# Kernel optimization log

Hardware: AMD Instinct MI355X
Metric: run time of the kernel (lower is better)

## Reference

```python
import jax, jax.numpy as jnp
import numpy as np
from jax import lax

IN_CH, HID, OUT_CH, N_MID, BATCH = 16, 8, 4, 60, 4194304


def setup_inputs() -> dict:
    key = jax.random.key(0)
    ks = jax.random.split(key, 7)
    scale = 1.0 / jnp.sqrt(jnp.float32(HID))  # keep 62-layer linear chain numerically stable
    x = jax.random.normal(ks[0], (BATCH, IN_CH), dtype=jnp.float32)
    W1 = jax.random.normal(ks[1], (HID, IN_CH), dtype=jnp.float32) * scale
    b1 = jax.random.normal(ks[2], (HID,), dtype=jnp.float32) * 0.01
    Ws = jax.random.normal(ks[3], (N_MID, HID, HID), dtype=jnp.float32) * scale
    bs = jax.random.normal(ks[4], (N_MID, HID), dtype=jnp.float32) * 0.01
    W2 = jax.random.normal(ks[5], (OUT_CH, HID), dtype=jnp.float32) * scale
    b2 = jax.random.normal(ks[6], (OUT_CH,), dtype=jnp.float32) * 0.01
    return {"x": x, "W1": W1, "b1": b1, "Ws": Ws, "bs": bs, "W2": W2, "b2": b2}


def reference(x, W1, b1, Ws, bs, W2, b2):
    # fc1: [B,16] -> [B,8]  (torch Linear: x @ W.T + b)
    h = x @ W1.T + b1

    # 60 sequential 8x8 Linear layers, no activation; scan over layer axis
    def step(h, wb):
        w, b = wb
        return h @ w.T + b, None

    h, _ = lax.scan(step, h, (Ws, bs))

    # fc2: [B,8] -> [B,4]
    return h @ W2.T + b2
```

## Files before the change

### kernel.cpp

```cpp
#include <hip/hip_runtime.h>

#define IN_CH  16
#define HID    8
#define OUT_CH 4
#define N_MID  60
#define BATCH  4194304

__global__ __launch_bounds__(128) void fold_kernel(
    const float* __restrict__ W1, const float* __restrict__ b1,
    const float* __restrict__ Ws, const float* __restrict__ bs,
    const float* __restrict__ W2, const float* __restrict__ b2,
    float* __restrict__ Mc ) {

    __shared__ float sWs[N_MID * HID * HID];
    __shared__ float sbs[N_MID * HID];
    __shared__ float A[2][HID][IN_CH];
    __shared__ float d[2][HID];

    const int t   = threadIdx.x;
    const int r   = t >> 4;
    const int col = t & 15;

    for (int i = t; i < N_MID * HID * HID; i += 128) sWs[i] = Ws[i];
    for (int i = t; i < N_MID * HID;       i += 128) sbs[i] = bs[i];

    A[0][r][col] = W1[r * IN_CH + col];
    if (t < HID) d[0][t] = b1[t];
    __syncthreads();

    int cur = 0;
    for (int l = 0; l < N_MID; ++l) {
        const float* W = sWs + l * HID * HID;
        float acc = 0.f;
        #pragma unroll
        for (int k = 0; k < HID; ++k)
            acc += W[r * HID + k] * A[cur][k][col];
        A[1 - cur][r][col] = acc;
        if (t < HID) {
            float bc = sbs[l * HID + t];
            #pragma unroll
            for (int k = 0; k < HID; ++k)
                bc += W[t * HID + k] * d[cur][k];
            d[1 - cur][t] = bc;
        }
        cur = 1 - cur;
        __syncthreads();
    }

    if (t < OUT_CH * IN_CH) {
        const int rr = t >> 4, cc = t & 15;
        float acc = 0.f;
        #pragma unroll
        for (int k = 0; k < HID; ++k)
            acc += W2[rr * HID + k] * A[cur][k][cc];
        Mc[rr * IN_CH + cc] = acc;
    }
    if (t < OUT_CH) {
        float acc = b2[t];
        #pragma unroll
        for (int k = 0; k < HID; ++k)
            acc += W2[t * HID + k] * d[cur][k];
        Mc[OUT_CH * IN_CH + t] = acc;
    }
}

__global__ __launch_bounds__(256) void apply_kernel(
    const float* __restrict__ x,
    const float* __restrict__ Mc,
    float* __restrict__ out) {

    const int tid = threadIdx.x;
    const size_t g = (size_t)blockIdx.x * 256 + tid;
    const int q = tid & 3;

    const float4* M4 = (const float4*)Mc;
    const float4 m0 = M4[0 * 4 + q];
    const float4 m1 = M4[1 * 4 + q];
    const float4 m2 = M4[2 * 4 + q];
    const float4 m3 = M4[3 * 4 + q];
    const float  cb = Mc[OUT_CH * IN_CH + q];

    const float4 xv = ((const float4*)x)[g];

    float p0 = m0.x * xv.x + m0.y * xv.y + m0.z * xv.z + m0.w * xv.w;
    float p1 = m1.x * xv.x + m1.y * xv.y + m1.z * xv.z + m1.w * xv.w;
    float p2 = m2.x * xv.x + m2.y * xv.y + m2.z * xv.z + m2.w * xv.w;
    float p3 = m3.x * xv.x + m3.y * xv.y + m3.z * xv.z + m3.w * xv.w;

    p0 += __shfl_xor(p0, 1); p1 += __shfl_xor(p1, 1);
    p2 += __shfl_xor(p2, 1); p3 += __shfl_xor(p3, 1);
    p0 += __shfl_xor(p0, 2); p1 += __shfl_xor(p1, 2);
    p2 += __shfl_xor(p2, 2); p3 += __shfl_xor(p3, 2);

    const float val = (q == 0 ? p0 : q == 1 ? p1 : q == 2 ? p2 : p3) + cb;
    out[g] = val;
}

extern "C" void kernel_launch(void* const* d_in, const int* in_sizes, int n_in,
                              void* d_out, int out_size, void* d_ws, size_t ws_size,
                              hipStream_t stream) {
    const float* x  = (const float*)d_in[0];
    const float* W1 = (const float*)d_in[1];
    const float* b1 = (const float*)d_in[2];
    const float* Ws = (const float*)d_in[3];
    const float* bs = (const float*)d_in[4];
    const float* W2 = (const float*)d_in[5];
    const float* b2 = (const float*)d_in[6];
    float* out = (float*)d_out;
    float* Mc  = (float*)d_ws;

    fold_kernel<<<1, 128, 0, stream>>>(W1, b1, Ws, bs, W2, b2, Mc);

    const int blocks = (BATCH * (IN_CH / 4)) / 256;
    apply_kernel<<<blocks, 256, 0, stream>>>(x, Mc, out);
}
```

Measured before the change: 396.0 us.

## Batch loads per thread, use nontemporal memory ops, reduce shuffles, shrink fold block

The apply kernel now handles 8 float4 elements per thread, spaced by a grid-wide stride, and issues all of their loads up front to keep more memory traffic in flight. Loads and stores use nontemporal hints so the streaming data does not pollute the cache. The shuffle reduction is replaced by a butterfly exchange-and-select scheme that needs 3 shuffles instead of 8. The fold kernel shrinks to a single 64-thread wavefront that copies weights to shared memory with float4 loads and computes two rows per thread; this cuts occupancy headroom but removes cross-wave synchronisation cost.

Result: no change. 395.6 us (-0.1%).

```diff
diff --git a/kernel.cpp b/kernel.cpp
--- a/kernel.cpp
+++ b/kernel.cpp
@@ -6,7 +6,9 @@
 #define N_MID  60
 #define BATCH  4194304
 
-__global__ __launch_bounds__(128) void fold_kernel(
+typedef float vfloat4 __attribute__((ext_vector_type(4)));
+
+__global__ __launch_bounds__(64) void fold_kernel(
     const float* __restrict__ W1, const float* __restrict__ b1,
     const float* __restrict__ Ws, const float* __restrict__ bs,
     const float* __restrict__ W2, const float* __restrict__ b2,
@@ -18,36 +20,49 @@
     __shared__ float d[2][HID];
 
     const int t   = threadIdx.x;
-    const int r   = t >> 4;
     const int col = t & 15;
+    const int r0  = t >> 4;
 
-    for (int i = t; i < N_MID * HID * HID; i += 128) sWs[i] = Ws[i];
-    for (int i = t; i < N_MID * HID;       i += 128) sbs[i] = bs[i];
+    {
+        const float4* Ws4  = (const float4*)Ws;
+        float4*       sW4  = (float4*)sWs;
+        #pragma unroll 1
+        for (int i = t; i < N_MID * HID * HID / 4; i += 64) sW4[i] = Ws4[i];
+        const float4* bs4  = (const float4*)bs;
+        float4*       sb4  = (float4*)sbs;
+        for (int i = t; i < N_MID * HID / 4; i += 64) sb4[i] = bs4[i];
+    }
 
-    A[0][r][col] = W1[r * IN_CH + col];
+    A[0][r0][col]     = W1[r0 * IN_CH + col];
+    A[0][r0 + 4][col] = W1[(r0 + 4) * IN_CH + col];
     if (t < HID) d[0][t] = b1[t];
     __syncthreads();
 
     int cur = 0;
     for (int l = 0; l < N_MID; ++l) {
         const float* W = sWs + l * HID * HID;
-        float acc = 0.f;
+        float a0 = 0.f, a1 = 0.f;
         #pragma unroll
-        for (int k = 0; k < HID; ++k)
-            acc += W[r * HID + k] * A[cur][k][col];
-        A[1 - cur][r][col] = acc;
+        for (int k = 0; k < HID; ++k) {
+            const float av = A[cur][k][col];
+            a0 += W[r0 * HID + k]       * av;
+            a1 += W[(r0 + 4) * HID + k] * av;
+        }
+        float bc = 0.f;
         if (t < HID) {
-            float bc = sbs[l * HID + t];
+            bc = sbs[l * HID + t];
             #pragma unroll
             for (int k = 0; k < HID; ++k)
                 bc += W[t * HID + k] * d[cur][k];
-            d[1 - cur][t] = bc;
         }
-        cur = 1 - cur;
+        A[1 - cur][r0][col]     = a0;
+        A[1 - cur][r0 + 4][col] = a1;
+        if (t < HID) d[1 - cur][t] = bc;
+        cur ^= 1;
         __syncthreads();
     }
 
-    if (t < OUT_CH * IN_CH) {
+    {
         const int rr = t >> 4, cc = t & 15;
         float acc = 0.f;
         #pragma unroll
@@ -64,14 +79,15 @@
     }
 }
 
+#define ITERS 8
+
 __global__ __launch_bounds__(256) void apply_kernel(
     const float* __restrict__ x,
     const float* __restrict__ Mc,
     float* __restrict__ out) {
 
     const int tid = threadIdx.x;
-    const size_t g = (size_t)blockIdx.x * 256 + tid;
-    const int q = tid & 3;
+    const int q   = tid & 3;
 
     const float4* M4 = (const float4*)Mc;
     const float4 m0 = M4[0 * 4 + q];
@@ -80,20 +96,38 @@
     const float4 m3 = M4[3 * 4 + q];
     const float  cb = Mc[OUT_CH * IN_CH + q];
 
-    const float4 xv = ((const float4*)x)[g];
+    const vfloat4* __restrict__ x4 = (const vfloat4*)x;
+    const size_t g0     = (size_t)blockIdx.x * 256 + tid;
+    const size_t stride = (size_t)gridDim.x * 256;
 
-    float p0 = m0.x * xv.x + m0.y * xv.y + m0.z * xv.z + m0.w * xv.w;
-    float p1 = m1.x * xv.x + m1.y * xv.y + m1.z * xv.z + m1.w * xv.w;
-    float p2 = m2.x * xv.x + m2.y * xv.y + m2.z * xv.z + m2.w * xv.w;
-    float p3 = m3.x * xv.x + m3.y * xv.y + m3.z * xv.z + m3.w * xv.w;
+    vfloat4 xv[ITERS];
+    #pragma unroll
+    for (int j = 0; j < ITERS; ++j)
+        xv[j] = __builtin_nontemporal_load(&x4[g0 + j * stride]);
 
-    p0 += __shfl_xor(p0, 1); p1 += __shfl_xor(p1, 1);
-    p2 += __shfl_xor(p2, 1); p3 += __shfl_xor(p3, 1);
-    p0 += __shfl_xor(p0, 2); p1 += __shfl_xor(p1, 2);
-    p2 += __shfl_xor(p2, 2); p3 += __shfl_xor(p3, 2);
+    const bool hi2 = (q & 2) != 0;
+    const bool lo1 = (q & 1) != 0;
 
-    const float val = (q == 0 ? p0 : q == 1 ? p1 : q == 2 ? p2 : p3) + cb;
-    out[g] = val;
+    #pragma unroll
+    for (int j = 0; j < ITERS; ++j) {
+        const vfloat4 v = xv[j];
+        float p0 = m0.x * v.x + m0.y * v.y + m0.z * v.z + m0.w * v.w;
+        float p1 = m1.x * v.x + m1.y * v.y + m1.z * v.z + m1.w * v.w;
+        float p2 = m2.x * v.x + m2.y * v.y + m2.z * v.z + m2.w * v.w;
+        float p3 = m3.x * v.x + m3.y * v.y + m3.z * v.z + m3.w * v.w;
+
+        float send_a = hi2 ? p0 : p2;
+        float send_b = hi2 ? p1 : p3;
+        float recv_a = __shfl_xor(send_a, 2);
+        float recv_b = __shfl_xor(send_b, 2);
+        float k0 = (hi2 ? p2 : p0) + recv_a;
+        float k1 = (hi2 ? p3 : p1) + recv_b;
+        float send = lo1 ? k0 : k1;
+        float recv = __shfl_xor(send, 1);
+        float val  = (lo1 ? k1 : k0) + recv + cb;
+
+        __builtin_nontemporal_store(val, &out[g0 + j * stride]);
+    }
 }
 
 extern "C" void kernel_launch(void* const* d_in, const int* in_sizes, int n_in,
@@ -109,8 +143,8 @@
     float* out = (float*)d_out;
     float* Mc  = (float*)d_ws;
 
-    fold_kernel<<<1, 128, 0, stream>>>(W1, b1, Ws, bs, W2, b2, Mc);
+    fold_kernel<<<1, 64, 0, stream>>>(W1, b1, Ws, bs, W2, b2, Mc);
 
-    const int blocks = (BATCH * (IN_CH / 4)) / 256;
+    const int blocks = (BATCH * (IN_CH / 4)) / (256 * ITERS);
     apply_kernel<<<blocks, 256, 0, stream>>>(x, Mc, out);
 }
```
